# Kernel optimization log

Measured on AMD Instinct MI355X. Metric: run time of the kernel, lower is better.

## Reference

```python
import jax, jax.numpy as jnp
import numpy as np

V = 10000   # vocab size
H = 768     # HIDDEN_SIZE
B = 8       # batch
S = 512     # padded seq len
L = 8       # TRANSFORMER_LAYERS
EPS = 1e-5  # torch LayerNorm default eps


def setup_inputs() -> dict:
    key = jax.random.key(0)
    ks = jax.random.split(key, 16)
    init = lambda k, shape: jax.random.normal(k, shape, jnp.float32) * 0.02
    x = jax.random.randint(ks[0], (B, S), 0, V)
    # full-length sequences: avoids NaN from the original's softmax(dim=1) over
    # fully -inf padded columns (same behavior as torch for this input)
    lengths = jnp.full((B,), S, dtype=jnp.int32)
    return {
        'x': x,
        'lengths': lengths,
        'emb_w': init(ks[1], (V, H)),
        'Wq': init(ks[2], (L, H, H)), 'bq': jnp.zeros((L, H), jnp.float32),
        'Wk': init(ks[3], (L, H, H)), 'bk': jnp.zeros((L, H), jnp.float32),
        'Wv': init(ks[4], (L, H, H)), 'bv': jnp.zeros((L, H), jnp.float32),
        'W1': init(ks[5], (L, H, H)), 'b1': jnp.zeros((L, H), jnp.float32),
        'W2': init(ks[6], (L, H, H)), 'b2': jnp.zeros((L, H), jnp.float32),
        'g1': jnp.ones((L, H), jnp.float32), 'be1': jnp.zeros((L, H), jnp.float32),
        'g2': jnp.ones((L, H), jnp.float32), 'be2': jnp.zeros((L, H), jnp.float32),
        'fc_w': init(ks[7], (H, H)), 'fc_b': jnp.zeros((H,), jnp.float32),
    }


def _layernorm(x, g, b):
    m = jnp.mean(x, axis=-1, keepdims=True)
    v = jnp.mean(jnp.square(x - m), axis=-1, keepdims=True)
    return (x - m) * jax.lax.rsqrt(v + EPS) * g + b


def _pos_encoding(seq, dim):
    pos = jnp.arange(seq, dtype=jnp.float32)[:, None]
    div = jnp.exp(jnp.arange(0, dim, 2, dtype=jnp.float32) * (-np.log(10000.0) / dim))
    ang = pos * div[None, :]                                  # [S, H/2]
    return jnp.stack([jnp.sin(ang), jnp.cos(ang)], axis=-1).reshape(seq, dim)


def reference(x, lengths, emb_w, Wq, bq, Wk, bk, Wv, bv, W1, b1, W2, b2,
              g1, be1, g2, be2, fc_w, fc_b):
    z = emb_w[x] + _pos_encoding(S, H)[None]                  # [B,S,H]
    causal = jnp.tril(jnp.ones((S, S), bool))                 # [S,S]
    valid = jnp.arange(S)[None, :] < lengths[:, None]         # [B,S]
    mask = causal[None] & valid[:, None, :] & valid[:, :, None]  # [B,S,S]
    scale = 1.0 / jnp.sqrt(jnp.float32(H))
    for i in range(L):
        q = z @ Wq[i] + bq[i]
        k = z @ Wk[i] + bk[i]
        v = z @ Wv[i] + bv[i]
        scores = jnp.einsum('bqh,bkh->bqk', q, k) * scale
        scores = jnp.where(mask, scores, -jnp.inf)
        # NOTE: original code applies softmax over dim=1 (query axis) — faithful
        atten = jax.nn.softmax(scores, axis=1)
        out = jnp.einsum('bqk,bkh->bqh', atten, v)
        o1 = _layernorm(z + out, g1[i], be1[i])               # eval: dropout=identity
        mid = jax.nn.relu(o1 @ W1[i] + b1[i]) @ W2[i] + b2[i]
        z = _layernorm(mid + o1, g2[i], be2[i])
    zf = z @ fc_w + fc_b                                      # [B,S,H]
    logits = jnp.einsum('bsh,vh->bsv', zf, emb_w)             # [B,S,V]
    return jax.nn.softmax(logits, axis=-1)
```

## Files before the change

kernel.cpp:

```cpp
#include <hip/hip_runtime.h>
#include <math.h>

typedef unsigned int   u32;
typedef unsigned short u16;
typedef __attribute__((ext_vector_type(8))) short bf16x8;
typedef __attribute__((ext_vector_type(4))) float f32x4;
typedef __attribute__((ext_vector_type(4))) unsigned short u16x4;

#define HID   768
#define SEQ   512
#define BATCH 8
#define LAYERS 8
#define VOC   10000
#define NROWS (BATCH*SEQ)
#define NH    ((long long)NROWS*HID)
#define SS8   ((long long)BATCH*SEQ*SEQ)
#define EPSLN 1e-5f
#define WSZ   ((long long)HID*HID)

__device__ __forceinline__ u16 f2bf(float f) {
    u32 u = __builtin_bit_cast(u32, f);
    return (u16)((u + 0x7fffu + ((u >> 16) & 1u)) >> 16);
}

__device__ __forceinline__ void async16(u16* lds, const u16* g) {
    __builtin_amdgcn_global_load_lds(
        (const __attribute__((address_space(1))) u32*)g,
        (__attribute__((address_space(3))) u32*)lds, 16, 0, 0);
}

__global__ __launch_bounds__(256) void embed_kernel(
    const int* __restrict__ x, const float* __restrict__ emb,
    float* __restrict__ Z, u16* __restrict__ Zh)
{
    const int row = blockIdx.x;
    const int s   = row & (SEQ - 1);
    const int tok = x[row];
    const long long base  = (long long)row * HID;
    const long long ebase = (long long)tok * HID;
    const float coef = -0.0239852613853544f;
    #pragma unroll
    for (int j = 0; j < 3; ++j) {
        const int h = threadIdx.x + 256 * j;
        const int i = h >> 1;
        const float ang = (float)s * expf((float)i * coef);
        const float pe  = (h & 1) ? cosf(ang) : sinf(ang);
        const float v = emb[ebase + h] + pe;
        Z[base + h]  = v;
        Zh[base + h] = f2bf(v);
    }
}

__global__ __launch_bounds__(256) void convert_emb(
    const float* __restrict__ e, u16* __restrict__ eh)
{
    const long long i = ((long long)blockIdx.x * 256 + threadIdx.x) * 4;
    const float4 v = *(const float4*)&e[i];
    u16x4 p;
    p[0] = f2bf(v.x); p[1] = f2bf(v.y); p[2] = f2bf(v.z); p[3] = f2bf(v.w);
    *(u16x4*)&eh[i] = p;
}

__global__ __launch_bounds__(256) void transp_all(
    const float* __restrict__ Wq, const float* __restrict__ Wk,
    const float* __restrict__ Wv, const float* __restrict__ W1,
    const float* __restrict__ W2, const float* __restrict__ fcw,
    u16* __restrict__ WT)
{
    __shared__ u16 tile[32][34];
    const int z = blockIdx.z;
    const float* src;
    long long doff;
    if (z < 40) {
        const int lyr = z / 5, idx = z % 5;
        const float* bases[5] = {Wq, Wk, Wv, W1, W2};
        src  = bases[idx] + (long long)lyr * WSZ;
        doff = ((long long)lyr * 5 + idx) * WSZ;
    } else {
        src = fcw; doff = 40LL * WSZ;
    }
    u16* D = WT + doff;
    const int n0 = blockIdx.x * 32, k0 = blockIdx.y * 32;
    const int c = threadIdx.x & 31, r0 = threadIdx.x >> 5;
    #pragma unroll
    for (int p = 0; p < 4; ++p)
        tile[r0 + 8*p][c] = f2bf(src[(long long)(k0 + r0 + 8*p) * HID + n0 + c]);
    __syncthreads();
    #pragma unroll
    for (int p = 0; p < 4; ++p)
        D[(long long)(n0 + r0 + 8*p) * HID + k0 + c] = tile[c][r0 + 8*p];
}

__global__ void pack_bias_all(const float* __restrict__ bq,
                              const float* __restrict__ bk,
                              const float* __restrict__ bv,
                              float* __restrict__ dst)
{
    const int part = blockIdx.x, l = blockIdx.y, h = threadIdx.x;
    const float* src = part == 0 ? bq : (part == 1 ? bk : bv);
    dst[((long long)l*3 + part) * HID + h] = src[(long long)l*HID + h];
}

template<int BM, int BN, int WM, int WN, bool RELU, bool OUT_BF16, bool XISM, bool VSPLIT>
__global__ __launch_bounds__(WM*WN*64) void gemm_mfma(
    const u16* __restrict__ A, int lda, long long sA,
    const u16* __restrict__ B, int ldb, long long sB,
    void* __restrict__ Cp, int ldc, long long sC,
    int N, int K, const float* __restrict__ bias, float alpha,
    u16* __restrict__ vt)
{
    constexpr int NW  = WM * WN;
    constexpr int MI  = BM / WM / 16;
    constexpr int NI  = BN / WN / 16;
    constexpr int APW = BM / 16 / NW;
    constexpr int BPW = BN / 16 / NW;
    constexpr int LPT = APW + BPW;
    __shared__ u16 As[2][BM * 32];
    __shared__ u16 Bs[2][BN * 32];
    const int bz = blockIdx.z;
    const int m0 = (XISM ? blockIdx.x : blockIdx.y) * BM;
    const int n0 = (XISM ? blockIdx.y : blockIdx.x) * BN;
    const int t = threadIdx.x, w = t >> 6, l = t & 63;
    const int lrow = l >> 2, lk8 = (l & 3) * 8;
    const int wm = (w / WN) * (BM / WM);
    const int wn = (w % WN) * (BN / WN);
    A += sA * bz; B += sB * bz;

    f32x4 acc[MI][NI];
    #pragma unroll
    for (int mi = 0; mi < MI; ++mi)
        #pragma unroll
        for (int ni = 0; ni < NI; ++ni) acc[mi][ni] = (f32x4){0.f,0.f,0.f,0.f};

    auto stage = [&](int buf, int k0) {
        #pragma unroll
        for (int r = 0; r < APW; ++r) {
            const int seg = w * APW + r;
            async16(&As[buf][seg * 512],
                    A + (long long)(m0 + seg*16 + lrow) * lda + (k0 + lk8));
        }
        #pragma unroll
        for (int r = 0; r < BPW; ++r) {
            const int seg = w * BPW + r;
            int row = n0 + seg*16 + lrow;
            row = row < N ? row : N - 1;
            async16(&Bs[buf][seg * 512], B + (long long)row * ldb + (k0 + lk8));
        }
    };
    const int fr = l & 15, fk = (l >> 4) * 8;
    auto compute = [&](int cur) {
        bf16x8 af[MI], bfr[NI];
        #pragma unroll
        for (int mi = 0; mi < MI; ++mi)
            af[mi] = *(const bf16x8*)&As[cur][(wm + mi*16 + fr) * 32 + fk];
        #pragma unroll
        for (int ni = 0; ni < NI; ++ni)
            bfr[ni] = *(const bf16x8*)&Bs[cur][(wn + ni*16 + fr) * 32 + fk];
        #pragma unroll
        for (int mi = 0; mi < MI; ++mi)
            #pragma unroll
            for (int ni = 0; ni < NI; ++ni)
                acc[mi][ni] = __builtin_amdgcn_mfma_f32_16x16x32_bf16(
                    af[mi], bfr[ni], acc[mi][ni], 0, 0, 0);
    };

    const int NS = K >> 5;
    stage(0, 0);
    for (int tt = 0; tt < NS; ++tt) {
        if (tt + 1 < NS) {
            stage((tt + 1) & 1, (tt + 1) << 5);
            asm volatile("s_waitcnt vmcnt(%0)\n\ts_barrier" :: "i"(LPT) : "memory");
        } else {
            asm volatile("s_waitcnt vmcnt(0)\n\ts_barrier" ::: "memory");
        }
        compute(tt & 1);
        asm volatile("s_barrier" ::: "memory");
    }

    float* Cf = (float*)Cp + sC * bz;
    u16*   Ch = (u16*)Cp + sC * bz;
    const int fq = l >> 4;
    #pragma unroll
    for (int ni = 0; ni < NI; ++ni) {
        const int col = n0 + wn + ni*16 + fr;
        const bool ok = col < N;
        const float bv = (bias && ok) ? bias[col] : 0.f;
        #pragma unroll
        for (int mi = 0; mi < MI; ++mi) {
            const int row0 = m0 + wm + mi*16 + fq*4;
            if constexpr (VSPLIT) {
                if (col < 1536) {
                    #pragma unroll
                    for (int v = 0; v < 4; ++v)
                        Ch[(long long)(row0 + v) * ldc + col] =
                            f2bf(alpha * acc[mi][ni][v] + bv);
                } else {
                    const int b9 = row0 >> 9, s9 = row0 & 511;
                    u16x4 pk;
                    #pragma unroll
                    for (int v = 0; v < 4; ++v)
                        pk[v] = f2bf(alpha * acc[mi][ni][v] + bv);
                    *(u16x4*)&vt[((long long)b9 * HID + (col - 1536)) * SEQ + s9] = pk;
                }
            } else {
                #pragma unroll
                for (int v = 0; v < 4; ++v) {
                    float val = alpha * acc[mi][ni][v] + bv;
                    if (RELU) val = fmaxf(val, 0.f);
                    if (ok) {
                        if (OUT_BF16) Ch[(long long)(row0 + v) * ldc + col] = f2bf(val);
                        else          Cf[(long long)(row0 + v) * ldc + col] = val;
                    }
                }
            }
        }
    }
}

__global__ __launch_bounds__(256) void gemm_conv(
    const u16* __restrict__ A, const float* __restrict__ Bf,
    float* __restrict__ C)
{
    __shared__ u16 As[128 * 32];
    __shared__ u16 Bs[128 * 32];
    const int m0 = blockIdx.x * 128;
    const int n0 = blockIdx.y * 128;
    const int t = threadIdx.x, w = t >> 6, l = t & 63;
    const int lrow = l >> 2, lk8 = (l & 3) * 8;
    const int wm = (w >> 1) * 64, wn = (w & 1) * 64;
    f32x4 acc[4][4];
    #pragma unroll
    for (int mi = 0; mi < 4; ++mi)
        #pragma unroll
        for (int ni = 0; ni < 4; ++ni) acc[mi][ni] = (f32x4){0.f,0.f,0.f,0.f};

    for (int k0 = 0; k0 < HID; k0 += 32) {
        #pragma unroll
        for (int r = 0; r < 2; ++r) {
            const int seg = w * 2 + r;
            async16(&As[seg * 512],
                    A + (long long)(m0 + seg*16 + lrow) * HID + (k0 + lk8));
        }
        #pragma unroll
        for (int r = 0; r < 2; ++r) {
            const int flat = r * 2048 + t * 8;
            int row = n0 + (flat >> 5);
            row = row < VOC ? row : VOC - 1;
            const float* g = Bf + (long long)row * HID + (k0 + (flat & 31));
            const float4 v0 = *(const float4*)g;
            const float4 v1 = *(const float4*)(g + 4);
            bf16x8 hv;
            hv[0]=(short)f2bf(v0.x); hv[1]=(short)f2bf(v0.y);
            hv[2]=(short)f2bf(v0.z); hv[3]=(short)f2bf(v0.w);
            hv[4]=(short)f2bf(v1.x); hv[5]=(short)f2bf(v1.y);
            hv[6]=(short)f2bf(v1.z); hv[7]=(short)f2bf(v1.w);
            *(bf16x8*)&Bs[flat] = hv;
        }
        __syncthreads();
        const int fr = l & 15, fk = (l >> 4) * 8;
        bf16x8 af[4], bfr[4];
        #pragma unroll
        for (int mi = 0; mi < 4; ++mi)
            af[mi] = *(const bf16x8*)&As[(wm + mi*16 + fr) * 32 + fk];
        #pragma unroll
        for (int ni = 0; ni < 4; ++ni)
            bfr[ni] = *(const bf16x8*)&Bs[(wn + ni*16 + fr) * 32 + fk];
        #pragma unroll
        for (int mi = 0; mi < 4; ++mi)
            #pragma unroll
            for (int ni = 0; ni < 4; ++ni)
                acc[mi][ni] = __builtin_amdgcn_mfma_f32_16x16x32_bf16(
                    af[mi], bfr[ni], acc[mi][ni], 0, 0, 0);
        __syncthreads();
    }
    const int fr = l & 15, fq = l >> 4;
    #pragma unroll
    for (int ni = 0; ni < 4; ++ni) {
        const int col = n0 + wn + ni*16 + fr;
        if (col >= VOC) continue;
        #pragma unroll
        for (int mi = 0; mi < 4; ++mi) {
            const int row0 = m0 + wm + mi*16 + fq*4;
            #pragma unroll
            for (int v = 0; v < 4; ++v)
                C[(long long)(row0 + v) * VOC + col] = acc[mi][ni][v];
        }
    }
}

__global__ __launch_bounds__(256) void softmax_q_kernel(
    const float* __restrict__ sc, u16* __restrict__ att,
    const int* __restrict__ lengths)
{
    const int b  = blockIdx.x;
    const int k0 = blockIdx.y * 16;
    const int tx = threadIdx.x & 15;
    const int ty = threadIdx.x >> 4;
    const int c  = k0 + tx;
    const int len = lengths[b];
    const float* base  = sc  + (long long)b * SEQ * SEQ;
    u16*         obase = att + (long long)b * SEQ * SEQ;
    const bool cvalid = (c < len);

    float m = -3.0e38f, ssum = 0.f;
    for (int q = ty; q < SEQ; q += 16) {
        if (cvalid && c <= q && q < len) {
            const float xv = base[(long long)q * SEQ + c];
            if (xv > m) { ssum = ssum * __expf(m - xv) + 1.f; m = xv; }
            else        { ssum += __expf(xv - m); }
        }
    }
    __shared__ float ms[16][17], ss[16][17];
    ms[ty][tx] = m; ss[ty][tx] = ssum;
    __syncthreads();
    if (ty == 0) {
        float M = ms[0][tx];
        #pragma unroll
        for (int r = 1; r < 16; ++r) M = fmaxf(M, ms[r][tx]);
        float Sx = 0.f;
        #pragma unroll
        for (int r = 0; r < 16; ++r) Sx += ss[r][tx] * __expf(ms[r][tx] - M);
        ms[0][tx] = M; ss[0][tx] = Sx;
    }
    __syncthreads();
    const float M   = ms[0][tx];
    const float den = ss[0][tx];
    const float inv = (den > 0.f) ? 1.f / den : 0.f;
    for (int q = ty; q < SEQ; q += 16) {
        const long long idx = (long long)q * SEQ + c;
        float o = 0.f;
        if (cvalid && c <= q && q < len) o = __expf(base[idx] - M) * inv;
        obase[idx] = f2bf(o);
    }
}

__global__ __launch_bounds__(256) void ln_add_kernel(
    const float* __restrict__ Xa, const float* __restrict__ Xb,
    float* __restrict__ O, u16* __restrict__ Oh,
    const float* __restrict__ g, const float* __restrict__ be)
{
    const int row = blockIdx.x;
    const long long base = (long long)row * HID;
    const int t = threadIdx.x;
    const float x0 = Xa[base + t]       + Xb[base + t];
    const float x1 = Xa[base + t + 256] + Xb[base + t + 256];
    const float x2 = Xa[base + t + 512] + Xb[base + t + 512];
    __shared__ float r1[4], r2[4];
    float s = x0 + x1 + x2;
    #pragma unroll
    for (int o = 32; o; o >>= 1) s += __shfl_down(s, o, 64);
    if ((t & 63) == 0) r1[t >> 6] = s;
    __syncthreads();
    const float mean = (r1[0] + r1[1] + r1[2] + r1[3]) * (1.f / HID);
    const float d0 = x0 - mean, d1 = x1 - mean, d2 = x2 - mean;
    float v = d0*d0 + d1*d1 + d2*d2;
    #pragma unroll
    for (int o = 32; o; o >>= 1) v += __shfl_down(v, o, 64);
    if ((t & 63) == 0) r2[t >> 6] = v;
    __syncthreads();
    const float var = (r2[0] + r2[1] + r2[2] + r2[3]) * (1.f / HID);
    const float rs = rsqrtf(var + EPSLN);
    const float y0 = d0 * rs * g[t]       + be[t];
    const float y1 = d1 * rs * g[t + 256] + be[t + 256];
    const float y2 = d2 * rs * g[t + 512] + be[t + 512];
    O[base + t]        = y0;  Oh[base + t]       = f2bf(y0);
    O[base + t + 256]  = y1;  Oh[base + t + 256] = f2bf(y1);
    O[base + t + 512]  = y2;  Oh[base + t + 512] = f2bf(y2);
}

__global__ __launch_bounds__(256) void softmax_v_kernel(float* __restrict__ out)
{
    __shared__ float row[VOC];
    __shared__ float rm[4], rs_[4];
    float4* o4 = (float4*)(out + (long long)blockIdx.x * VOC);
    const int t = threadIdx.x;
    float m = -3.0e38f, s = 0.f;
    for (int i = t; i < VOC/4; i += 256) {
        const float4 v = o4[i];
        *(float4*)&row[i*4] = v;
        #pragma unroll
        for (int j = 0; j < 4; ++j) {
            const float xv = j==0?v.x:(j==1?v.y:(j==2?v.z:v.w));
            const float d = xv - m;
            if (d > 0.f) { s = s * __expf(-d) + 1.f; m = xv; }
            else         { s += __expf(d); }
        }
    }
    #pragma unroll
    for (int o = 32; o; o >>= 1) {
        const float om = __shfl_down(m, o, 64), os = __shfl_down(s, o, 64);
        const float M = fmaxf(m, om);
        s = s * __expf(m - M) + os * __expf(om - M);
        m = M;
    }
    if ((t & 63) == 0) { rm[t >> 6] = m; rs_[t >> 6] = s; }
    __syncthreads();
    const float M = fmaxf(fmaxf(rm[0], rm[1]), fmaxf(rm[2], rm[3]));
    const float S = rs_[0]*__expf(rm[0]-M) + rs_[1]*__expf(rm[1]-M)
                  + rs_[2]*__expf(rm[2]-M) + rs_[3]*__expf(rm[3]-M);
    const float inv = 1.f / S;
    for (int i = t; i < VOC/4; i += 256) {
        float4 v = *(const float4*)&row[i*4];
        v.x = __expf(v.x - M) * inv;
        v.y = __expf(v.y - M) * inv;
        v.z = __expf(v.z - M) * inv;
        v.w = __expf(v.w - M) * inv;
        o4[i] = v;
    }
}

extern "C" void kernel_launch(void* const* d_in, const int* in_sizes, int n_in,
                              void* d_out, int out_size, void* d_ws, size_t ws_size,
                              hipStream_t stream)
{
    const int*   x    = (const int*)  d_in[0];
    const int*   lens = (const int*)  d_in[1];
    const float* emb  = (const float*)d_in[2];
    const float* Wq   = (const float*)d_in[3];
    const float* bq   = (const float*)d_in[4];
    const float* Wk   = (const float*)d_in[5];
    const float* bk   = (const float*)d_in[6];
    const float* Wv   = (const float*)d_in[7];
    const float* bv   = (const float*)d_in[8];
    const float* W1   = (const float*)d_in[9];
    const float* b1   = (const float*)d_in[10];
    const float* W2   = (const float*)d_in[11];
    const float* b2   = (const float*)d_in[12];
    const float* g1   = (const float*)d_in[13];
    const float* be1  = (const float*)d_in[14];
    const float* g2   = (const float*)d_in[15];
    const float* be2  = (const float*)d_in[16];
    const float* fcw  = (const float*)d_in[17];
    const float* fcb  = (const float*)d_in[18];

    float* out = (float*)d_out;
    float* Zb     = out;
    float* O1f    = Zb + NH;
    float* M2f    = O1f + NH;
    float* SCORES = M2f + NH;
    float* BQKV   = SCORES + SS8;
    u16* ub   = (u16*)(BQKV + (long long)LAYERS * 2304);
    u16* Zbh  = ub;  ub += NH;
    u16* QKVh = ub;  ub += (long long)NROWS * 1536;
    u16* ATTB = ub;  ub += SS8;
    u16* Vt   = ub;  ub += NH;
    u16* O1h  = ub;  ub += NH;
    u16* M1h  = ub;  ub += NH;
    u16* WT   = ub;  ub += 41LL * WSZ;

    u16* ZFh = (u16*)d_ws;
    u16* EH  = ZFh + NH;
    const bool ehpath = ws_size >= (size_t)((NH + (long long)VOC * HID) * 2);

    const float scale = 1.0f / sqrtf((float)HID);
    const dim3 blk(256), blk128(128);

    embed_kernel<<<NROWS, blk, 0, stream>>>(x, emb, Zb, Zbh);
    transp_all<<<dim3(24, 24, 41), blk, 0, stream>>>(Wq, Wk, Wv, W1, W2, fcw, WT);
    pack_bias_all<<<dim3(3, LAYERS), dim3(768), 0, stream>>>(bq, bk, bv, BQKV);
    if (ehpath) convert_emb<<<7500, blk, 0, stream>>>(emb, EH);

    for (int l = 0; l < LAYERS; ++l) {
        const u16* wl = WT + (long long)l * 5 * WSZ;

        gemm_mfma<128,128,2,2, false, true, false, true><<<dim3(18, 32), blk, 0, stream>>>(
            Zbh, HID, 0, wl, HID, 0, QKVh, 1536, 0,
            2304, HID, BQKV + (long long)l * 2304, 1.0f, Vt);

        gemm_mfma<64,64,2,1, false, false, false, false><<<dim3(8, 8, BATCH), blk128, 0, stream>>>(
            QKVh, 1536, (long long)SEQ * 1536,
            QKVh + 768, 1536, (long long)SEQ * 1536,
            SCORES, SEQ, (long long)SEQ * SEQ,
            SEQ, HID, nullptr, scale, nullptr);

        softmax_q_kernel<<<dim3(BATCH, SEQ/16), blk, 0, stream>>>(SCORES, ATTB, lens);

        gemm_mfma<64,64,2,1, false, false, false, false><<<dim3(12, 8, BATCH), blk128, 0, stream>>>(
            ATTB, SEQ, (long long)SEQ * SEQ,
            Vt, SEQ, (long long)HID * SEQ,
            O1f, HID, (long long)SEQ * HID,
            HID, SEQ, nullptr, 1.0f, nullptr);

        ln_add_kernel<<<NROWS, blk, 0, stream>>>(Zb, O1f, O1f, O1h,
                                                 g1 + l*HID, be1 + l*HID);
        gemm_mfma<64,64,2,1, true, true, false, false><<<dim3(12, 64), blk128, 0, stream>>>(
            O1h, HID, 0, wl + 3*WSZ, HID, 0, M1h, HID, 0,
            HID, HID, b1 + l*HID, 1.0f, nullptr);
        gemm_mfma<64,64,2,1, false, false, false, false><<<dim3(12, 64), blk128, 0, stream>>>(
            M1h, HID, 0, wl + 4*WSZ, HID, 0, M2f, HID, 0,
            HID, HID, b2 + l*HID, 1.0f, nullptr);
        ln_add_kernel<<<NROWS, blk, 0, stream>>>(M2f, O1f, Zb, Zbh,
                                                 g2 + l*HID, be2 + l*HID);
    }

    gemm_mfma<64,64,2,1, false, true, false, false><<<dim3(12, 64), blk128, 0, stream>>>(
        Zbh, HID, 0, WT + 40LL*WSZ, HID, 0, ZFh, HID, 0,
        HID, HID, fcb, 1.0f, nullptr);

    if (ehpath) {
        gemm_mfma<128,128,2,2, false, false, true, false><<<dim3(32, 79), blk, 0, stream>>>(
            ZFh, HID, 0, EH, HID, 0, out, VOC, 0,
            VOC, HID, nullptr, 1.0f, nullptr);
    } else {
        gemm_conv<<<dim3(32, 79), blk, 0, stream>>>(ZFh, emb, out);
    }

    softmax_v_kernel<<<NROWS, blk, 0, stream>>>(out);
}
```

Before: 1.248 ms.

## Add swizzled 64x64 BK64 GEMM, bf16 logits, register-cached query softmax

Adds a new 64x64 GEMM kernel with a 64-wide K step and XOR-swizzled LDS layout, used for the attention and MLP GEMMs, and pins the main MFMA kernel to 128x128 tiles. The vocab logits GEMM now writes bf16 into the upper half of each fp32 output row, and the vocab softmax reads those bf16 values, which halves logit write and read traffic. The query-axis softmax keeps its 32 values per thread in registers so scores are not re-read from global memory. The risks are lower logit precision from bf16 rounding and in-place aliasing of the bf16 logits with the fp32 output buffer.

```diff
diff --git a/kernel.cpp b/kernel.cpp
--- a/kernel.cpp
+++ b/kernel.cpp
@@ -6,6 +6,7 @@
 typedef __attribute__((ext_vector_type(8))) short bf16x8;
 typedef __attribute__((ext_vector_type(4))) float f32x4;
 typedef __attribute__((ext_vector_type(4))) unsigned short u16x4;
+typedef __attribute__((ext_vector_type(8))) unsigned short u16x8;
 
 #define HID   768
 #define SEQ   512
@@ -21,6 +22,9 @@
 __device__ __forceinline__ u16 f2bf(float f) {
     u32 u = __builtin_bit_cast(u32, f);
     return (u16)((u + 0x7fffu + ((u >> 16) & 1u)) >> 16);
+}
+__device__ __forceinline__ float bf2f(u16 h) {
+    return __builtin_bit_cast(float, (u32)h << 16);
 }
 
 __device__ __forceinline__ void async16(u16* lds, const u16* g) {
@@ -101,47 +105,40 @@
     dst[((long long)l*3 + part) * HID + h] = src[(long long)l*HID + h];
 }
 
-template<int BM, int BN, int WM, int WN, bool RELU, bool OUT_BF16, bool XISM, bool VSPLIT>
-__global__ __launch_bounds__(WM*WN*64) void gemm_mfma(
+template<bool RELU, bool OUT_BF16, bool XISM, bool VSPLIT>
+__global__ __launch_bounds__(256) void gemm_mfma(
     const u16* __restrict__ A, int lda, long long sA,
     const u16* __restrict__ B, int ldb, long long sB,
     void* __restrict__ Cp, int ldc, long long sC,
     int N, int K, const float* __restrict__ bias, float alpha,
     u16* __restrict__ vt)
 {
-    constexpr int NW  = WM * WN;
-    constexpr int MI  = BM / WM / 16;
-    constexpr int NI  = BN / WN / 16;
-    constexpr int APW = BM / 16 / NW;
-    constexpr int BPW = BN / 16 / NW;
-    constexpr int LPT = APW + BPW;
-    __shared__ u16 As[2][BM * 32];
-    __shared__ u16 Bs[2][BN * 32];
+    __shared__ u16 As[2][128 * 32];
+    __shared__ u16 Bs[2][128 * 32];
     const int bz = blockIdx.z;
-    const int m0 = (XISM ? blockIdx.x : blockIdx.y) * BM;
-    const int n0 = (XISM ? blockIdx.y : blockIdx.x) * BN;
+    const int m0 = (XISM ? blockIdx.x : blockIdx.y) * 128;
+    const int n0 = (XISM ? blockIdx.y : blockIdx.x) * 128;
     const int t = threadIdx.x, w = t >> 6, l = t & 63;
     const int lrow = l >> 2, lk8 = (l & 3) * 8;
-    const int wm = (w / WN) * (BM / WM);
-    const int wn = (w % WN) * (BN / WN);
+    const int wm = (w >> 1) * 64, wn = (w & 1) * 64;
     A += sA * bz; B += sB * bz;
 
-    f32x4 acc[MI][NI];
-    #pragma unroll
-    for (int mi = 0; mi < MI; ++mi)
-        #pragma unroll
-        for (int ni = 0; ni < NI; ++ni) acc[mi][ni] = (f32x4){0.f,0.f,0.f,0.f};
+    f32x4 acc[4][4];
+    #pragma unroll
+    for (int mi = 0; mi < 4; ++mi)
+        #pragma unroll
+        for (int ni = 0; ni < 4; ++ni) acc[mi][ni] = (f32x4){0.f,0.f,0.f,0.f};
 
     auto stage = [&](int buf, int k0) {
         #pragma unroll
-        for (int r = 0; r < APW; ++r) {
-            const int seg = w * APW + r;
+        for (int r = 0; r < 2; ++r) {
+            const int seg = w * 2 + r;
             async16(&As[buf][seg * 512],
                     A + (long long)(m0 + seg*16 + lrow) * lda + (k0 + lk8));
         }
         #pragma unroll
-        for (int r = 0; r < BPW; ++r) {
-            const int seg = w * BPW + r;
+        for (int r = 0; r < 2; ++r) {
+            const int seg = w * 2 + r;
             int row = n0 + seg*16 + lrow;
             row = row < N ? row : N - 1;
             async16(&Bs[buf][seg * 512], B + (long long)row * ldb + (k0 + lk8));
@@ -149,17 +146,17 @@
     };
     const int fr = l & 15, fk = (l >> 4) * 8;
     auto compute = [&](int cur) {
-        bf16x8 af[MI], bfr[NI];
-        #pragma unroll
-        for (int mi = 0; mi < MI; ++mi)
+        bf16x8 af[4], bfr[4];
+        #pragma unroll
+        for (int mi = 0; mi < 4; ++mi)
             af[mi] = *(const bf16x8*)&As[cur][(wm + mi*16 + fr) * 32 + fk];
         #pragma unroll
-        for (int ni = 0; ni < NI; ++ni)
+        for (int ni = 0; ni < 4; ++ni)
             bfr[ni] = *(const bf16x8*)&Bs[cur][(wn + ni*16 + fr) * 32 + fk];
         #pragma unroll
-        for (int mi = 0; mi < MI; ++mi)
+        for (int mi = 0; mi < 4; ++mi)
             #pragma unroll
-            for (int ni = 0; ni < NI; ++ni)
+            for (int ni = 0; ni < 4; ++ni)
                 acc[mi][ni] = __builtin_amdgcn_mfma_f32_16x16x32_bf16(
                     af[mi], bfr[ni], acc[mi][ni], 0, 0, 0);
     };
@@ -169,7 +166,7 @@
     for (int tt = 0; tt < NS; ++tt) {
         if (tt + 1 < NS) {
             stage((tt + 1) & 1, (tt + 1) << 5);
-            asm volatile("s_waitcnt vmcnt(%0)\n\ts_barrier" :: "i"(LPT) : "memory");
+            asm volatile("s_waitcnt vmcnt(4)\n\ts_barrier" ::: "memory");
         } else {
             asm volatile("s_waitcnt vmcnt(0)\n\ts_barrier" ::: "memory");
         }
@@ -181,12 +178,12 @@
     u16*   Ch = (u16*)Cp + sC * bz;
     const int fq = l >> 4;
     #pragma unroll
-    for (int ni = 0; ni < NI; ++ni) {
+    for (int ni = 0; ni < 4; ++ni) {
         const int col = n0 + wn + ni*16 + fr;
         const bool ok = col < N;
         const float bv = (bias && ok) ? bias[col] : 0.f;
         #pragma unroll
-        for (int mi = 0; mi < MI; ++mi) {
+        for (int mi = 0; mi < 4; ++mi) {
             const int row0 = m0 + wm + mi*16 + fq*4;
             if constexpr (VSPLIT) {
                 if (col < 1536) {
@@ -217,9 +214,104 @@
     }
 }
 
+template<bool RELU, bool OUT_BF16>
+__global__ __launch_bounds__(128) void gemm_small(
+    const u16* __restrict__ A, int lda, long long sA,
+    const u16* __restrict__ B, int ldb, long long sB,
+    void* __restrict__ Cp, int ldc, long long sC,
+    int N, int K, const float* __restrict__ bias, float alpha)
+{
+    __shared__ u16 As[2][64 * 64];
+    __shared__ u16 Bs[2][64 * 64];
+    const int bz = blockIdx.z;
+    const int n0 = blockIdx.x * 64;
+    const int m0 = blockIdx.y * 64;
+    const int t = threadIdx.x, w = t >> 6, l = t & 63;
+    const int srow = l >> 3;
+    const int skof = ((l & 7) ^ srow) * 8;
+    const int wm = w * 32;
+    A += sA * bz; B += sB * bz;
+
+    f32x4 acc[2][4];
+    #pragma unroll
+    for (int mi = 0; mi < 2; ++mi)
+        #pragma unroll
+        for (int ni = 0; ni < 4; ++ni) acc[mi][ni] = (f32x4){0.f,0.f,0.f,0.f};
+
+    auto stage = [&](int buf, int k0) {
+        #pragma unroll
+        for (int r = 0; r < 4; ++r) {
+            const int seg = w * 4 + r;
+            const int row = seg * 8 + srow;
+            async16(&As[buf][seg * 512],
+                    A + (long long)(m0 + row) * lda + (k0 + skof));
+        }
+        #pragma unroll
+        for (int r = 0; r < 4; ++r) {
+            const int seg = w * 4 + r;
+            const int row = seg * 8 + srow;
+            async16(&Bs[buf][seg * 512],
+                    B + (long long)(n0 + row) * ldb + (k0 + skof));
+        }
+    };
+    const int fr = l & 15, fkb = l >> 4;
+    auto compute = [&](int cur) {
+        #pragma unroll
+        for (int ks = 0; ks < 2; ++ks) {
+            const int ps = ((ks * 4 + fkb) ^ (fr & 7)) * 8;
+            bf16x8 af[2], bfv[4];
+            #pragma unroll
+            for (int mi = 0; mi < 2; ++mi)
+                af[mi] = *(const bf16x8*)&As[cur][(wm + mi*16 + fr) * 64 + ps];
+            #pragma unroll
+            for (int ni = 0; ni < 4; ++ni)
+                bfv[ni] = *(const bf16x8*)&Bs[cur][(ni*16 + fr) * 64 + ps];
+            #pragma unroll
+            for (int mi = 0; mi < 2; ++mi)
+                #pragma unroll
+                for (int ni = 0; ni < 4; ++ni)
+                    acc[mi][ni] = __builtin_amdgcn_mfma_f32_16x16x32_bf16(
+                        af[mi], bfv[ni], acc[mi][ni], 0, 0, 0);
+        }
+    };
+
+    const int NS = K >> 6;
+    stage(0, 0);
+    for (int tt = 0; tt < NS; ++tt) {
+        if (tt + 1 < NS) {
+            stage((tt + 1) & 1, (tt + 1) << 6);
+            asm volatile("s_waitcnt vmcnt(8)\n\ts_barrier" ::: "memory");
+        } else {
+            asm volatile("s_waitcnt vmcnt(0)\n\ts_barrier" ::: "memory");
+        }
+        compute(tt & 1);
+        asm volatile("s_barrier" ::: "memory");
+    }
+
+    float* Cf = (float*)Cp + sC * bz;
+    u16*   Ch = (u16*)Cp + sC * bz;
+    const int fq = l >> 4;
+    #pragma unroll
+    for (int ni = 0; ni < 4; ++ni) {
+        const int col = n0 + ni*16 + fr;
+        const float bv = bias ? bias[col] : 0.f;
+        #pragma unroll
+        for (int mi = 0; mi < 2; ++mi) {
+            const int row0 = m0 + wm + mi*16 + fq*4;
+            #pragma unroll
+            for (int v = 0; v < 4; ++v) {
+                float val = alpha * acc[mi][ni][v] + bv;
+                if (RELU) val = fmaxf(val, 0.f);
+                if (OUT_BF16) Ch[(long long)(row0 + v) * ldc + col] = f2bf(val);
+                else          Cf[(long long)(row0 + v) * ldc + col] = val;
+            }
+        }
+    }
+}
+
 __global__ __launch_bounds__(256) void gemm_conv(
     const u16* __restrict__ A, const float* __restrict__ Bf,
-    float* __restrict__ C)
+    u16* __restrict__ C)
 {
     __shared__ u16 As[128 * 32];
     __shared__ u16 Bs[128 * 32];
@@ -283,7 +375,7 @@
             const int row0 = m0 + wm + mi*16 + fq*4;
             #pragma unroll
             for (int v = 0; v < 4; ++v)
-                C[(long long)(row0 + v) * VOC + col] = acc[mi][ni][v];
+                C[(long long)(row0 + v) * (2*VOC) + col] = f2bf(acc[mi][ni][v]);
         }
     }
 }
@@ -302,13 +394,17 @@
     u16*         obase = att + (long long)b * SEQ * SEQ;
     const bool cvalid = (c < len);
 
+    float vals[32];
     float m = -3.0e38f, ssum = 0.f;
-    for (int q = ty; q < SEQ; q += 16) {
-        if (cvalid && c <= q && q < len) {
-            const float xv = base[(long long)q * SEQ + c];
-            if (xv > m) { ssum = ssum * __expf(m - xv) + 1.f; m = xv; }
-            else        { ssum += __expf(xv - m); }
-        }
+    #pragma unroll
+    for (int i = 0; i < 32; ++i) {
+        const int q = ty + 16 * i;
+        float xv = -3.0e38f;
+        if (cvalid && c <= q && q < len)
+            xv = base[(long long)q * SEQ + c];
+        vals[i] = xv;
+        if (xv > m) { ssum = ssum * __expf(m - xv) + 1.f; m = xv; }
+        else if (xv > -3.0e38f) { ssum += __expf(xv - m); }
     }
     __shared__ float ms[16][17], ss[16][17];
     ms[ty][tx] = m; ss[ty][tx] = ssum;
@@ -326,11 +422,10 @@
     const float M   = ms[0][tx];
     const float den = ss[0][tx];
     const float inv = (den > 0.f) ? 1.f / den : 0.f;
-    for (int q = ty; q < SEQ; q += 16) {
-        const long long idx = (long long)q * SEQ + c;
-        float o = 0.f;
-        if (cvalid && c <= q && q < len) o = __expf(base[idx] - M) * inv;
-        obase[idx] = f2bf(o);
+    #pragma unroll
+    for (int i = 0; i < 32; ++i) {
+        const int q = ty + 16 * i;
+        obase[(long long)q * SEQ + c] = f2bf(__expf(vals[i] - M) * inv);
     }
 }
 
@@ -372,15 +467,16 @@
 {
     __shared__ float row[VOC];
     __shared__ float rm[4], rs_[4];
-    float4* o4 = (float4*)(out + (long long)blockIdx.x * VOC);
+    const long long obase = (long long)blockIdx.x * VOC;
+    const u16* lg = (const u16*)out + 2 * obase + VOC;
     const int t = threadIdx.x;
     float m = -3.0e38f, s = 0.f;
-    for (int i = t; i < VOC/4; i += 256) {
-        const float4 v = o4[i];
-        *(float4*)&row[i*4] = v;
-        #pragma unroll
-        for (int j = 0; j < 4; ++j) {
-            const float xv = j==0?v.x:(j==1?v.y:(j==2?v.z:v.w));
+    for (int i = t * 8; i < VOC; i += 2048) {
+        const u16x8 h8 = *(const u16x8*)&lg[i];
+        #pragma unroll
+        for (int j = 0; j < 8; ++j) {
+            const float xv = bf2f(h8[j]);
+            row[i + j] = xv;
             const float d = xv - m;
             if (d > 0.f) { s = s * __expf(-d) + 1.f; m = xv; }
             else         { s += __expf(d); }
@@ -399,13 +495,13 @@
     const float S = rs_[0]*__expf(rm[0]-M) + rs_[1]*__expf(rm[1]-M)
                   + rs_[2]*__expf(rm[2]-M) + rs_[3]*__expf(rm[3]-M);
     const float inv = 1.f / S;
-    for (int i = t; i < VOC/4; i += 256) {
-        float4 v = *(const float4*)&row[i*4];
+    for (int i = t * 4; i < VOC; i += 1024) {
+        float4 v = *(const float4*)&row[i];
         v.x = __expf(v.x - M) * inv;
         v.y = __expf(v.y - M) * inv;
         v.z = __expf(v.z - M) * inv;
         v.w = __expf(v.w - M) * inv;
-        o4[i] = v;
+        *(float4*)&out[obase + i] = v;
     }
 }
 
@@ -451,6 +547,7 @@
     u16* ZFh = (u16*)d_ws;
     u16* EH  = ZFh + NH;
     const bool ehpath = ws_size >= (size_t)((NH + (long long)VOC * HID) * 2);
+    u16* LOGH = (u16*)out + VOC;
 
     const float scale = 1.0f / sqrtf((float)HID);
     const dim3 blk(256), blk128(128);
@@ -463,46 +560,46 @@
     for (int l = 0; l < LAYERS; ++l) {
         const u16* wl = WT + (long long)l * 5 * WSZ;
 
-        gemm_mfma<128,128,2,2, false, true, false, true><<<dim3(18, 32), blk, 0, stream>>>(
+        gemm_mfma<false, true, false, true><<<dim3(18, 32), blk, 0, stream>>>(
             Zbh, HID, 0, wl, HID, 0, QKVh, 1536, 0,
             2304, HID, BQKV + (long long)l * 2304, 1.0f, Vt);
 
-        gemm_mfma<64,64,2,1, false, false, false, false><<<dim3(8, 8, BATCH), blk128, 0, stream>>>(
+        gemm_small<false, false><<<dim3(8, 8, BATCH), blk128, 0, stream>>>(
             QKVh, 1536, (long long)SEQ * 1536,
             QKVh + 768, 1536, (long long)SEQ * 1536,
             SCORES, SEQ, (long long)SEQ * SEQ,
-            SEQ, HID, nullptr, scale, nullptr);
+            512, HID, nullptr, scale);
 
         softmax_q_kernel<<<dim3(BATCH, SEQ/16), blk, 0, stream>>>(SCORES, ATTB, lens);
 
-        gemm_mfma<64,64,2,1, false, false, false, false><<<dim3(12, 8, BATCH), blk128, 0, stream>>>(
+        gemm_small<false, false><<<dim3(12, 8, BATCH), blk128, 0, stream>>>(
             ATTB, SEQ, (long long)SEQ * SEQ,
             Vt, SEQ, (long long)HID * SEQ,
             O1f, HID, (long long)SEQ * HID,
-            HID, SEQ, nullptr, 1.0f, nullptr);
+            768, SEQ, nullptr, 1.0f);
 
         ln_add_kernel<<<NROWS, blk, 0, stream>>>(Zb, O1f, O1f, O1h,
                                                  g1 + l*HID, be1 + l*HID);
-        gemm_mfma<64,64,2,1, true, true, false, false><<<dim3(12, 64), blk128, 0, stream>>>(
+        gemm_small<true, true><<<dim3(12, 64), blk128, 0, stream>>>(
             O1h, HID, 0, wl + 3*WSZ, HID, 0, M1h, HID, 0,
-            HID, HID, b1 + l*HID, 1.0f, nullptr);
-        gemm_mfma<64,64,2,1, false, false, false, false><<<dim3(12, 64), blk128, 0, stream>>>(
+            768, HID, b1 + l*HID, 1.0f);
+        gemm_small<false, false><<<dim3(12, 64), blk128, 0, stream>>>(
             M1h, HID, 0, wl + 4*WSZ, HID, 0, M2f, HID, 0,
-            HID, HID, b2 + l*HID, 1.0f, nullptr);
+            768, HID, b2 + l*HID, 1.0f);
         ln_add_kernel<<<NROWS, blk, 0, stream>>>(M2f, O1f, Zb, Zbh,
                                                  g2 + l*HID, be2 + l*HID);
     }
 
-    gemm_mfma<64,64,2,1, false, true, false, false><<<dim3(12, 64), blk128, 0, stream>>>(
+    gemm_small<false, true><<<dim3(12, 64), blk128, 0, stream>>>(
         Zbh, HID, 0, WT + 40LL*WSZ, HID, 0, ZFh, HID, 0,
-        HID, HID, fcb, 1.0f, nullptr);
+        768, HID, fcb, 1.0f);
 
     if (ehpath) {
-        gemm_mfma<128,128,2,2, false, false, true, false><<<dim3(32, 79), blk, 0, stream>>>(
-            ZFh, HID, 0, EH, HID, 0, out, VOC, 0,
+        gemm_mfma<false, true, true, false><<<dim3(32, 79), blk, 0, stream>>>(
+            ZFh, HID, 0, EH, HID, 0, LOGH, 2*VOC, 0,
             VOC, HID, nullptr, 1.0f, nullptr);
     } else {
-        gemm_conv<<<dim3(32, 79), blk, 0, stream>>>(ZFh, emb, out);
+        gemm_conv<<<dim3(32, 79), blk, 0, stream>>>(ZFh, emb, LOGH);
     }
 
     softmax_v_kernel<<<NROWS, blk, 0, stream>>>(out);
```

Measured after the change: 1.095 ms. -12.2%, faster.
